# Kernel optimization log

Measured on AMD Instinct MI355X. Metric: run time of the kernel, lower is better.

## Reference

```python
import jax, jax.numpy as jnp
import numpy as np

SR = 32000
N_FFT = 1024
HOP = 320
N_MELS = 128
PCEN_EPS = 1e-6
LN_EPS = 1e-6


def _hz_to_mel(f):
    return 2595.0 * np.log10(1.0 + f / 700.0)


def _mel_to_hz(m):
    return 700.0 * (10.0 ** (m / 2595.0) - 1.0)


def make_mel_fb():
    # HTK-scale triangular mel filterbank, [n_freqs, n_mels] (torchaudio default)
    n_freqs = N_FFT // 2 + 1
    mels = np.linspace(_hz_to_mel(0.0), _hz_to_mel(SR / 2.0), N_MELS + 2)
    f_pts = _mel_to_hz(mels)                       # [n_mels+2]
    all_freqs = np.linspace(0.0, SR / 2.0, n_freqs)
    f_diff = f_pts[1:] - f_pts[:-1]
    slopes = f_pts[None, :] - all_freqs[:, None]   # [n_freqs, n_mels+2]
    down = -slopes[:, :-2] / f_diff[:-1]
    up = slopes[:, 2:] / f_diff[1:]
    fb = np.maximum(0.0, np.minimum(down, up))
    return fb.astype(np.float32)


def setup_inputs() -> dict:
    key = jax.random.key(0)
    x = jax.random.normal(key, (16, 320000), dtype=jnp.float32)
    return {
        "x": x,
        "mel_fb": jnp.asarray(make_mel_fb()),
        "log_s": jnp.asarray(np.log(0.025), dtype=jnp.float32),
        "log_alpha": jnp.asarray(np.log(0.98), dtype=jnp.float32),
        "log_delta": jnp.asarray(np.log(2.0), dtype=jnp.float32),
        "log_r": jnp.asarray(np.log(0.5), dtype=jnp.float32),
    }


def reference(x, mel_fb, log_s, log_alpha, log_delta, log_r):
    B, T = x.shape
    pad = N_FFT // 2
    xp = jnp.pad(x, ((0, 0), (pad, pad)), mode="reflect")
    n_frames = 1 + (xp.shape[1] - N_FFT) // HOP           # = T//HOP + 1
    idx = jnp.arange(n_frames)[:, None] * HOP + jnp.arange(N_FFT)[None, :]
    frames = xp[:, idx]                                    # [B, F, N_FFT]
    # periodic Hann window (torch.hann_window default)
    win = 0.5 * (1.0 - jnp.cos(2.0 * jnp.pi * jnp.arange(N_FFT) / N_FFT))
    spec = jnp.fft.rfft(frames * win, axis=-1)             # [B, F, N_FFT//2+1]
    power = spec.real ** 2 + spec.imag ** 2                # power spectrogram
    E = jnp.einsum("bfk,km->bfm", power, mel_fb)           # [B, F, M] mel energies

    s = jnp.exp(log_s)
    alpha = jnp.exp(log_alpha)
    delta = jnp.exp(log_delta)
    r = jnp.exp(log_r)

    # Causal exponential smoother M(t) = (1-s) M(t-1) + s E(t), M init = first frame
    E_t = jnp.swapaxes(E, 0, 1)                            # [F, B, M]

    def step(m, e):
        m = (1.0 - s) * m + s * e
        return m, m

    _, M_t = jax.lax.scan(step, E_t[0], E_t)
    smooth = jnp.swapaxes(M_t, 0, 1)                       # [B, F, M]

    pcen = (E / (PCEN_EPS + smooth) ** alpha + delta) ** r - delta ** r

    # affine-free layer_norm over last dim (n_mels), eps=1e-6
    mu = jnp.mean(pcen, axis=-1, keepdims=True)
    var = jnp.var(pcen, axis=-1, keepdims=True)
    return (pcen - mu) / jnp.sqrt(var + LN_EPS)
```

## Files before the change

kernel.cpp:

```cpp
#include <hip/hip_runtime.h>
#include <math.h>

#define SRATE   32000
#define NFFT    1024
#define HOP     320
#define NBINS   513
#define NMELS   128
#define NFRAMES 1001
#define NB      16
#define TLEN    320000
#define PCEN_EPS 1e-6f
#define LN_EPS   1e-6f
#define MAXW     64

#define CL      16
#define NCHUNK  63

__device__ __forceinline__ int P(int i) { return i + (i >> 3); }
#define ZPAD 1152

__global__ __launch_bounds__(256) void k_prep(
    const float* __restrict__ fb, int* __restrict__ kmin, int* __restrict__ klen,
    float* __restrict__ wv, float* __restrict__ win, float2* __restrict__ twg)
{
    const int blk = blockIdx.x;
    const int tid = threadIdx.x;
    if (blk < NMELS) {
        const int m = blk;
        __shared__ int smin[4], smax[4];
        int lmin = 1 << 30, lmax = -1;
        for (int k = tid; k < NBINS; k += 256) {
            if (fb[k * NMELS + m] > 0.f) {
                if (k < lmin) lmin = k;
                if (k > lmax) lmax = k;
            }
        }
        #pragma unroll
        for (int off = 32; off; off >>= 1) {
            int om = __shfl_xor(lmin, off); if (om < lmin) lmin = om;
            int ox = __shfl_xor(lmax, off); if (ox > lmax) lmax = ox;
        }
        if ((tid & 63) == 0) { smin[tid >> 6] = lmin; smax[tid >> 6] = lmax; }
        __syncthreads();
        int k0 = min(min(smin[0], smin[1]), min(smin[2], smin[3]));
        int k1 = max(max(smax[0], smax[1]), max(smax[2], smax[3]));
        int L  = (k1 < 0) ? 0 : min(k1 - k0 + 1, MAXW);
        if (tid == 0) { kmin[m] = (k1 < 0) ? 0 : k0; klen[m] = L; }
        if (tid < L) wv[m * MAXW + tid] = fb[(k0 + tid) * NMELS + m];
    } else {
        const int i = (blk - NMELS) * 256 + tid;
        if (i < NFFT) {
            float sp = sinpif((float)i * (1.0f / (float)NFFT));
            win[i] = sp * sp;
        } else if (i < NFFT + 256) {
            int n = i - NFFT;
            float sn, cn;
            sincospif((float)n * (1.0f / 512.0f), &sn, &cn);
            twg[n] = make_float2(cn, -sn);
        }
    }
}

__global__ __launch_bounds__(256, 4) void k_melspec(
    const float* __restrict__ x,
    const int*   __restrict__ kmin,
    const int*   __restrict__ klen,
    const float* __restrict__ wv,
    const float* __restrict__ fb,
    const float* __restrict__ win_g,
    const float2* __restrict__ twg,
    float* __restrict__ E,
    int usePacked)
{
    __shared__ float2 zA[2][ZPAD], zB[2][ZPAD];
    __shared__ float2 tws[256];

    const int tid = threadIdx.x;
    const int g   = blockIdx.x;

    if (usePacked) {
        tws[tid] = twg[tid];
    } else {
        float sn, cn;
        sincospif((float)tid * (1.0f / 512.0f), &sn, &cn);
        tws[tid] = make_float2(cn, -sn);
    }

    const int i0 = tid * 4;
    #pragma unroll
    for (int u = 0; u < 2; ++u) {
        const int fa = 4 * g + 2 * u;
        const int fbr = fa + 1;
        const int ba = fa / NFRAMES,  ta = fa  - ba * NFRAMES;
        const int bb = fbr / NFRAMES, tb = fbr - bb * NFRAMES;
        const float* xa = x + (size_t)ba * TLEN;
        const float* xb = x + (size_t)bb * TLEN;
        const int basea = ta * HOP - (NFFT / 2);
        const int baseb = tb * HOP - (NFFT / 2);
        const bool safe = usePacked &&
                          basea >= 0 && baseb >= 0 &&
                          (basea + NFFT - 1 < TLEN) && (baseb + NFFT - 1 < TLEN);
        if (safe) {
            float4 v0 = *(const float4*)(xa + basea + i0);
            float4 v1 = *(const float4*)(xb + baseb + i0);
            float4 w  = *(const float4*)(win_g + i0);
            zA[u][P(i0 + 0)] = make_float2(v0.x * w.x, v1.x * w.x);
            zA[u][P(i0 + 1)] = make_float2(v0.y * w.y, v1.y * w.y);
            zA[u][P(i0 + 2)] = make_float2(v0.z * w.z, v1.z * w.z);
            zA[u][P(i0 + 3)] = make_float2(v0.w * w.w, v1.w * w.w);
        } else {
            #pragma unroll
            for (int q = 0; q < 4; ++q) {
                const int i = i0 + q;
                int j0 = basea + i;
                j0 = (j0 < 0) ? -j0 : ((j0 >= TLEN) ? (2 * TLEN - 2 - j0) : j0);
                int j1 = baseb + i;
                j1 = (j1 < 0) ? -j1 : ((j1 >= TLEN) ? (2 * TLEN - 2 - j1) : j1);
                float w;
                if (usePacked) w = win_g[i];
                else { float sp = sinpif((float)i * (1.0f / (float)NFFT)); w = sp * sp; }
                zA[u][P(i)] = make_float2(xa[j0] * w, xb[j1] * w);
            }
        }
    }
    __syncthreads();

    float2 (*zs)[ZPAD] = zA;
    float2 (*zd)[ZPAD] = zB;
    #pragma unroll
    for (int st = 0; st < 5; ++st) {
        const int mm = 1 << (2 * st);
        const int n  = tid & ~(mm - 1);
        const int o  = (n << 2) | (tid & (mm - 1));
        float2 w1 = tws[n];
        const float c1 = w1.x, s1 = w1.y;
        const float c2 = c1 * c1 - s1 * s1, s2 = 2.f * c1 * s1;
        const float c3 = c1 * c2 - s1 * s2, s3 = c1 * s2 + s1 * c2;
        #pragma unroll
        for (int u = 0; u < 2; ++u) {
            float2 a0 = zs[u][P(tid)];
            float2 a1 = zs[u][P(tid + 256)];
            float2 a2 = zs[u][P(tid + 512)];
            float2 a3 = zs[u][P(tid + 768)];
            float t0r = a0.x + a2.x, t0i = a0.y + a2.y;
            float t1r = a0.x - a2.x, t1i = a0.y - a2.y;
            float t2r = a1.x + a3.x, t2i = a1.y + a3.y;
            float t3r = a1.y - a3.y, t3i = a3.x - a1.x;
            float y1r = t1r + t3r, y1i = t1i + t3i;
            float y2r = t0r - t2r, y2i = t0i - t2i;
            float y3r = t1r - t3r, y3i = t1i - t3i;
            zd[u][P(o)]          = make_float2(t0r + t2r,            t0i + t2i);
            zd[u][P(o + mm)]     = make_float2(y1r * c1 - y1i * s1,  y1r * s1 + y1i * c1);
            zd[u][P(o + 2 * mm)] = make_float2(y2r * c2 - y2i * s2,  y2r * s2 + y2i * c2);
            zd[u][P(o + 3 * mm)] = make_float2(y3r * c3 - y3i * s3,  y3r * s3 + y3i * c3);
        }
        __syncthreads();
        float2 (*tp)[ZPAD] = zs; zs = zd; zd = tp;
    }

    {
        const int u  = tid >> 7;
        const int kk = tid & 127;
        for (int k = kk; k < NBINS; k += 128) {
            float2 Z  = zs[u][P(k)];
            const int kr = (NFFT - k) & (NFFT - 1);
            float2 Zr = zs[u][P(kr)];
            float x1r = Z.x + Zr.x, x1i = Z.y - Zr.y;
            float x2r = Z.y + Zr.y, x2i = Zr.x - Z.x;
            zd[u][P(k)] = make_float2(0.25f * (x1r * x1r + x1i * x1i),
                                      0.25f * (x2r * x2r + x2i * x2i));
        }
    }
    __syncthreads();

    {
        const int u = tid >> 7;
        const int m = tid & 127;
        const int fa = 4 * g + 2 * u;
        float acc0 = 0.f, acc1 = 0.f;
        if (usePacked) {
            const int k0 = kmin[m], L = klen[m];
            const float* w = wv + m * MAXW;
            for (int j = 0; j < L; ++j) {
                float2 pk = zd[u][P(k0 + j)];
                float ww = w[j];
                acc0 += pk.x * ww; acc1 += pk.y * ww;
            }
        } else {
            for (int k = 0; k < NBINS; ++k) {
                float2 pk = zd[u][P(k)];
                float ww = fb[k * NMELS + m];
                acc0 += pk.x * ww; acc1 += pk.y * ww;
            }
        }
        E[(size_t)fa * NMELS + m]       = acc0;
        E[(size_t)(fa + 1) * NMELS + m] = acc1;
    }
}

__global__ __launch_bounds__(256) void k_pcen_chunk(
    const float* __restrict__ E, float* __restrict__ Bws,
    float* __restrict__ E0ws, const float* __restrict__ p_ls)
{
    const int gid = blockIdx.x * blockDim.x + threadIdx.x;
    const int m = gid & (NMELS - 1);
    const int c = (gid >> 7) % NCHUNK;
    const int b = gid / (NMELS * NCHUNK);

    const float s = expf(p_ls[0]);
    const float a = 1.f - s;

    const int t0 = c * CL;
    const int L  = (t0 + CL <= NFRAMES) ? CL : (NFRAMES - t0);
    const float* col = E + (size_t)b * NFRAMES * NMELS + m;

    if (c == 0) E0ws[b * NMELS + m] = col[0];

    float Bacc;
    if (L == CL) {
        float e[CL];
        #pragma unroll
        for (int j = 0; j < CL; ++j)
            e[j] = col[(size_t)(t0 + j) * NMELS];
        float p0 = 0.f, p1 = 0.f, p2 = 0.f, p3 = 0.f;
        #pragma unroll
        for (int u = 0; u < 4; ++u) {
            p0 = a * p0 + s * e[u];
            p1 = a * p1 + s * e[4 + u];
            p2 = a * p2 + s * e[8 + u];
            p3 = a * p3 + s * e[12 + u];
        }
        const float a2 = a * a, a4 = a2 * a2, a8 = a4 * a4, a12 = a8 * a4;
        Bacc = a12 * p0 + a8 * p1 + a4 * p2 + p3;
    } else {
        Bacc = 0.f;
        for (int j = 0; j < L; ++j)
            Bacc = a * Bacc + s * col[(size_t)(t0 + j) * NMELS];
    }
    Bws[gid] = Bacc;
}

__global__ __launch_bounds__(256) void k_pcen_ln(
    float* __restrict__ E, const float* __restrict__ Bws,
    const float* __restrict__ E0ws,
    const float* __restrict__ p_ls, const float* __restrict__ p_la,
    const float* __restrict__ p_ld, const float* __restrict__ p_lr)
{
    __shared__ float sm[2 * CL][NMELS];

    const int tid  = threadIdx.x;
    const int half = tid >> 7;
    const int m    = tid & 127;
    const int b    = blockIdx.x >> 5;
    const int cp   = blockIdx.x & 31;
    const int c    = cp * 2 + half;

    const float s     = expf(p_ls[0]);
    const float alpha = expf(p_la[0]);
    const float delta = expf(p_ld[0]);
    const float r     = expf(p_lr[0]);
    const float dr    = __powf(delta, r);
    const float a     = 1.f - s;
    const float a2 = a * a, a4 = a2 * a2, a8 = a4 * a4;
    const float a16 = a8 * a8;

    if (c < NCHUNK) {
        float M = E0ws[b * NMELS + m];
        const float* Bcol = Bws + (size_t)b * NCHUNK * NMELS + m;
        int cc = 0;
        for (; cc + 8 <= c; cc += 8) {
            float b0 = Bcol[(size_t)(cc + 0) * NMELS];
            float b1 = Bcol[(size_t)(cc + 1) * NMELS];
            float b2 = Bcol[(size_t)(cc + 2) * NMELS];
            float b3 = Bcol[(size_t)(cc + 3) * NMELS];
            float b4 = Bcol[(size_t)(cc + 4) * NMELS];
            float b5 = Bcol[(size_t)(cc + 5) * NMELS];
            float b6 = Bcol[(size_t)(cc + 6) * NMELS];
            float b7 = Bcol[(size_t)(cc + 7) * NMELS];
            M = a16 * M + b0; M = a16 * M + b1; M = a16 * M + b2; M = a16 * M + b3;
            M = a16 * M + b4; M = a16 * M + b5; M = a16 * M + b6; M = a16 * M + b7;
        }
        for (; cc < c; ++cc)
            M = a16 * M + Bcol[(size_t)cc * NMELS];

        const int t0 = c * CL;
        const int L  = (t0 + CL <= NFRAMES) ? CL : (NFRAMES - t0);
        const float* col = E + ((size_t)b * NFRAMES + t0) * NMELS + m;
        for (int j = 0; j < L; ++j) {
            float e = col[(size_t)j * NMELS];
            M = a * M + s * e;
            float den = __powf(PCEN_EPS + M, alpha);
            sm[half * CL + j][m] = __powf(e / den + delta, r) - dr;
        }
    }
    __syncthreads();

    const int wid  = tid >> 6;
    const int lane = tid & 63;
    for (int row = wid; row < 2 * CL; row += 4) {
        const int cc = cp * 2 + (row >> 4);
        if (cc >= NCHUNK) continue;
        const int j   = row & (CL - 1);
        const int tt0 = cc * CL;
        const int LL  = (tt0 + CL <= NFRAMES) ? CL : (NFRAMES - tt0);
        if (j >= LL) continue;
        float v0 = sm[row][lane], v1 = sm[row][lane + 64];
        float sum = v0 + v1;
        float sq  = v0 * v0 + v1 * v1;
        #pragma unroll
        for (int off = 32; off; off >>= 1) {
            sum += __shfl_xor(sum, off);
            sq  += __shfl_xor(sq,  off);
        }
        float mu  = sum * (1.f / 128.f);
        float var = sq * (1.f / 128.f) - mu * mu;
        float inv = rsqrtf(var + LN_EPS);
        float* p = E + ((size_t)b * NFRAMES + tt0 + j) * NMELS;
        p[lane]      = (v0 - mu) * inv;
        p[lane + 64] = (v1 - mu) * inv;
    }
}

__global__ __launch_bounds__(256) void k_pcen_serial(
    float* __restrict__ E,
    const float* __restrict__ p_ls, const float* __restrict__ p_la,
    const float* __restrict__ p_ld, const float* __restrict__ p_lr)
{
    const int gid = blockIdx.x * blockDim.x + threadIdx.x;
    const int b = gid >> 7;
    const int m = gid & 127;

    const float s     = expf(p_ls[0]);
    const float alpha = expf(p_la[0]);
    const float delta = expf(p_ld[0]);
    const float r     = expf(p_lr[0]);
    const float dr    = powf(delta, r);
    const float a     = 1.f - s;

    float* col = E + (size_t)b * NFRAMES * NMELS + m;
    float M = col[0];
    for (int t = 0; t < NFRAMES; ++t) {
        float e = col[(size_t)t * NMELS];
        M = a * M + s * e;
        float den = __powf(PCEN_EPS + M, alpha);
        float p   = __powf(e / den + delta, r) - dr;
        col[(size_t)t * NMELS] = p;
    }
}

__global__ __launch_bounds__(256) void k_ln(float* __restrict__ out) {
    const int wid  = threadIdx.x >> 6;
    const int lane = threadIdx.x & 63;
    const int row  = blockIdx.x * 4 + wid;
    float* p = out + (size_t)row * NMELS;
    float v0 = p[lane], v1 = p[lane + 64];
    float sum = v0 + v1;
    float sq  = v0 * v0 + v1 * v1;
    #pragma unroll
    for (int off = 32; off; off >>= 1) {
        sum += __shfl_xor(sum, off);
        sq  += __shfl_xor(sq,  off);
    }
    float mu  = sum * (1.f / 128.f);
    float var = sq * (1.f / 128.f) - mu * mu;
    float inv = rsqrtf(var + LN_EPS);
    p[lane]      = (v0 - mu) * inv;
    p[lane + 64] = (v1 - mu) * inv;
}

extern "C" void kernel_launch(void* const* d_in, const int* in_sizes, int n_in,
                              void* d_out, int out_size, void* d_ws, size_t ws_size,
                              hipStream_t stream) {
    const float* x   = (const float*)d_in[0];
    const float* fb  = (const float*)d_in[1];
    const float* lsp = (const float*)d_in[2];
    const float* lap = (const float*)d_in[3];
    const float* ldp = (const float*)d_in[4];
    const float* lrp = (const float*)d_in[5];
    float* out = (float*)d_out;

    const size_t packElems = 128 + 128 + 8192 + 1024 + 512;
    const size_t scanElems = (size_t)NB * NCHUNK * NMELS;
    const size_t needPack  = packElems * 4;
    const size_t needScan  = (packElems + scanElems + (size_t)NB * NMELS) * 4;

    int usePacked = (ws_size >= needPack) ? 1 : 0;
    int useScan   = (ws_size >= needScan) ? 1 : 0;

    int*    kmin = (int*)d_ws;
    int*    klen = kmin + NMELS;
    float*  wv   = (float*)(klen + NMELS);
    float*  win  = wv + (size_t)NMELS * MAXW;
    float2* twg  = (float2*)(win + NFFT);
    float*  Bws  = (float*)(twg + 256);
    float*  E0ws = Bws + scanElems;

    if (usePacked)
        k_prep<<<NMELS + 5, 256, 0, stream>>>(fb, kmin, klen, wv, win, twg);

    k_melspec<<<NB * NFRAMES / 4, 256, 0, stream>>>(
        x, kmin, klen, wv, fb, win, twg, out, usePacked);

    if (useScan) {
        const int nThread = NB * NCHUNK * NMELS;
        k_pcen_chunk<<<nThread / 256, 256, 0, stream>>>(out, Bws, E0ws, lsp);
        k_pcen_ln<<<NB * 32, 256, 0, stream>>>(out, Bws, E0ws, lsp, lap, ldp, lrp);
    } else {
        k_pcen_serial<<<(NB * NMELS) / 256, 256, 0, stream>>>(out, lsp, lap, ldp, lrp);
        k_ln<<<(NB * NFRAMES) / 4, 256, 0, stream>>>(out);
    }
}
```

Before: 82.30 us.

## Use in-place radix-4 DIF FFT with digit-reversal table to halve LDS

Replaces the out-of-place Stockham radix-4 FFT, which ping-ponged between two shared buffers, with an in-place decimation-in-frequency FFT on a single buffer. The last stage is split out because it needs no twiddles. A shared lookup table maps natural bin indices to the digit-reversed padded LDS positions for the real-split and mel stages. Halving the FFT shared memory lets launch bounds ask for 7 blocks per CU instead of 4, aiming to hide latency. The cost is an extra table build per block and indirect LDS reads during the post-processing and mel accumulation.

```diff
diff --git a/kernel.cpp b/kernel.cpp
--- a/kernel.cpp
+++ b/kernel.cpp
@@ -18,6 +18,11 @@
 
 __device__ __forceinline__ int P(int i) { return i + (i >> 3); }
 #define ZPAD 1152
+
+__device__ __forceinline__ int DR4(int e) {
+    return ((e & 3) << 8) | (((e >> 2) & 3) << 6) | (((e >> 4) & 3) << 4)
+         | (((e >> 6) & 3) << 2) | ((e >> 8) & 3);
+}
 
 __global__ __launch_bounds__(256) void k_prep(
     const float* __restrict__ fb, int* __restrict__ kmin, int* __restrict__ klen,
@@ -61,7 +66,7 @@
     }
 }
 
-__global__ __launch_bounds__(256, 4) void k_melspec(
+__global__ __launch_bounds__(256, 7) void k_melspec(
     const float* __restrict__ x,
     const int*   __restrict__ kmin,
     const int*   __restrict__ klen,
@@ -72,8 +77,9 @@
     float* __restrict__ E,
     int usePacked)
 {
-    __shared__ float2 zA[2][ZPAD], zB[2][ZPAD];
+    __shared__ float2 z[2][ZPAD];
     __shared__ float2 tws[256];
+    __shared__ unsigned short prt[1024];
 
     const int tid = threadIdx.x;
     const int g   = blockIdx.x;
@@ -85,6 +91,9 @@
         sincospif((float)tid * (1.0f / 512.0f), &sn, &cn);
         tws[tid] = make_float2(cn, -sn);
     }
+    #pragma unroll
+    for (int e = tid; e < 1024; e += 256)
+        prt[e] = (unsigned short)P(DR4(e));
 
     const int i0 = tid * 4;
     #pragma unroll
@@ -104,10 +113,10 @@
             float4 v0 = *(const float4*)(xa + basea + i0);
             float4 v1 = *(const float4*)(xb + baseb + i0);
             float4 w  = *(const float4*)(win_g + i0);
-            zA[u][P(i0 + 0)] = make_float2(v0.x * w.x, v1.x * w.x);
-            zA[u][P(i0 + 1)] = make_float2(v0.y * w.y, v1.y * w.y);
-            zA[u][P(i0 + 2)] = make_float2(v0.z * w.z, v1.z * w.z);
-            zA[u][P(i0 + 3)] = make_float2(v0.w * w.w, v1.w * w.w);
+            z[u][P(i0 + 0)] = make_float2(v0.x * w.x, v1.x * w.x);
+            z[u][P(i0 + 1)] = make_float2(v0.y * w.y, v1.y * w.y);
+            z[u][P(i0 + 2)] = make_float2(v0.z * w.z, v1.z * w.z);
+            z[u][P(i0 + 3)] = make_float2(v0.w * w.w, v1.w * w.w);
         } else {
             #pragma unroll
             for (int q = 0; q < 4; ++q) {
@@ -119,29 +128,28 @@
                 float w;
                 if (usePacked) w = win_g[i];
                 else { float sp = sinpif((float)i * (1.0f / (float)NFFT)); w = sp * sp; }
-                zA[u][P(i)] = make_float2(xa[j0] * w, xb[j1] * w);
+                z[u][P(i)] = make_float2(xa[j0] * w, xb[j1] * w);
             }
         }
     }
     __syncthreads();
 
-    float2 (*zs)[ZPAD] = zA;
-    float2 (*zd)[ZPAD] = zB;
     #pragma unroll
-    for (int st = 0; st < 5; ++st) {
-        const int mm = 1 << (2 * st);
-        const int n  = tid & ~(mm - 1);
-        const int o  = (n << 2) | (tid & (mm - 1));
+    for (int s = 0; s < 4; ++s) {
+        const int q    = 256 >> (2 * s);
+        const int k    = tid & (q - 1);
+        const int base = ((tid & ~(q - 1)) << 2) | k;
+        const int n    = k << (2 * s);
         float2 w1 = tws[n];
         const float c1 = w1.x, s1 = w1.y;
         const float c2 = c1 * c1 - s1 * s1, s2 = 2.f * c1 * s1;
         const float c3 = c1 * c2 - s1 * s2, s3 = c1 * s2 + s1 * c2;
         #pragma unroll
         for (int u = 0; u < 2; ++u) {
-            float2 a0 = zs[u][P(tid)];
-            float2 a1 = zs[u][P(tid + 256)];
-            float2 a2 = zs[u][P(tid + 512)];
-            float2 a3 = zs[u][P(tid + 768)];
+            float2 a0 = z[u][P(base)];
+            float2 a1 = z[u][P(base + q)];
+            float2 a2 = z[u][P(base + 2 * q)];
+            float2 a3 = z[u][P(base + 3 * q)];
             float t0r = a0.x + a2.x, t0i = a0.y + a2.y;
             float t1r = a0.x - a2.x, t1i = a0.y - a2.y;
             float t2r = a1.x + a3.x, t2i = a1.y + a3.y;
@@ -149,26 +157,46 @@
             float y1r = t1r + t3r, y1i = t1i + t3i;
             float y2r = t0r - t2r, y2i = t0i - t2i;
             float y3r = t1r - t3r, y3i = t1i - t3i;
-            zd[u][P(o)]          = make_float2(t0r + t2r,            t0i + t2i);
-            zd[u][P(o + mm)]     = make_float2(y1r * c1 - y1i * s1,  y1r * s1 + y1i * c1);
-            zd[u][P(o + 2 * mm)] = make_float2(y2r * c2 - y2i * s2,  y2r * s2 + y2i * c2);
-            zd[u][P(o + 3 * mm)] = make_float2(y3r * c3 - y3i * s3,  y3r * s3 + y3i * c3);
+            z[u][P(base)]         = make_float2(t0r + t2r,           t0i + t2i);
+            z[u][P(base + q)]     = make_float2(y1r * c1 - y1i * s1, y1r * s1 + y1i * c1);
+            z[u][P(base + 2 * q)] = make_float2(y2r * c2 - y2i * s2, y2r * s2 + y2i * c2);
+            z[u][P(base + 3 * q)] = make_float2(y3r * c3 - y3i * s3, y3r * s3 + y3i * c3);
         }
         __syncthreads();
-        float2 (*tp)[ZPAD] = zs; zs = zd; zd = tp;
+    }
+
+    {
+        const int base = tid << 2;
+        #pragma unroll
+        for (int u = 0; u < 2; ++u) {
+            float2 a0 = z[u][P(base)];
+            float2 a1 = z[u][P(base + 1)];
+            float2 a2 = z[u][P(base + 2)];
+            float2 a3 = z[u][P(base + 3)];
+            float t0r = a0.x + a2.x, t0i = a0.y + a2.y;
+            float t1r = a0.x - a2.x, t1i = a0.y - a2.y;
+            float t2r = a1.x + a3.x, t2i = a1.y + a3.y;
+            float t3r = a1.y - a3.y, t3i = a3.x - a1.x;
+            z[u][P(base)]     = make_float2(t0r + t2r, t0i + t2i);
+            z[u][P(base + 1)] = make_float2(t1r + t3r, t1i + t3i);
+            z[u][P(base + 2)] = make_float2(t0r - t2r, t0i - t2i);
+            z[u][P(base + 3)] = make_float2(t1r - t3r, t1i - t3i);
+        }
+        __syncthreads();
     }
 
     {
         const int u  = tid >> 7;
         const int kk = tid & 127;
-        for (int k = kk; k < NBINS; k += 128) {
-            float2 Z  = zs[u][P(k)];
-            const int kr = (NFFT - k) & (NFFT - 1);
-            float2 Zr = zs[u][P(kr)];
+        for (int k = kk; k < 513; k += 128) {
+            const int sk  = prt[k];
+            const int skr = prt[(NFFT - k) & (NFFT - 1)];
+            float2 Z  = z[u][sk];
+            float2 Zr = z[u][skr];
             float x1r = Z.x + Zr.x, x1i = Z.y - Zr.y;
             float x2r = Z.y + Zr.y, x2i = Zr.x - Z.x;
-            zd[u][P(k)] = make_float2(0.25f * (x1r * x1r + x1i * x1i),
-                                      0.25f * (x2r * x2r + x2i * x2i));
+            z[u][sk] = make_float2(0.25f * (x1r * x1r + x1i * x1i),
+                                   0.25f * (x2r * x2r + x2i * x2i));
         }
     }
     __syncthreads();
@@ -182,13 +210,13 @@
             const int k0 = kmin[m], L = klen[m];
             const float* w = wv + m * MAXW;
             for (int j = 0; j < L; ++j) {
-                float2 pk = zd[u][P(k0 + j)];
+                float2 pk = z[u][prt[k0 + j]];
                 float ww = w[j];
                 acc0 += pk.x * ww; acc1 += pk.y * ww;
             }
         } else {
             for (int k = 0; k < NBINS; ++k) {
-                float2 pk = zd[u][P(k)];
+                float2 pk = z[u][prt[k]];
                 float ww = fb[k * NMELS + m];
                 acc0 += pk.x * ww; acc1 += pk.y * ww;
             }
```

New measurement: 84.70 us. +2.9%, slower.

## Compute each FFT pair per wavefront with register radix-16 stages and swizzled LDS

Applied to the files above, without the earlier changes.

The 5-stage block-wide radix-4 FFT with a __syncthreads after every stage is replaced by a per-wavefront 1024-point FFT. Each 64-lane wave owns one frame pair and does two register-resident radix-16 passes plus a final radix-4 pass, using an XOR-swizzled LDS layout and a precomputed permutation table for bit-reversed output. Each block now handles 8 frames instead of 4, and block-level barriers are removed in favour of implicit wave-synchronous execution. The removed barriers rely on lockstep within a 64-wide wave with no explicit wave barrier, so correctness depends on compiler ordering of LDS accesses. Register pressure from the 16-element arrays may also limit occupancy.

```diff
diff --git a/kernel.cpp b/kernel.cpp
--- a/kernel.cpp
+++ b/kernel.cpp
@@ -16,8 +16,53 @@
 #define CL      16
 #define NCHUNK  63
 
-__device__ __forceinline__ int P(int i) { return i + (i >> 3); }
-#define ZPAD 1152
+__device__ __forceinline__ int SWZ(int i) {
+    return i ^ (((i >> 6) & 3) << 2) ^ ((i >> 4) & 3);
+}
+
+__device__ __forceinline__ float2 cmul(float2 a, float2 b) {
+    return make_float2(a.x * b.x - a.y * b.y, a.x * b.y + a.y * b.x);
+}
+
+__device__ __forceinline__ void r4(float2 a0, float2 a1, float2 a2, float2 a3,
+                                   float2& y0, float2& y1, float2& y2, float2& y3) {
+    float t0r = a0.x + a2.x, t0i = a0.y + a2.y;
+    float t1r = a0.x - a2.x, t1i = a0.y - a2.y;
+    float t2r = a1.x + a3.x, t2i = a1.y + a3.y;
+    float t3r = a1.y - a3.y, t3i = a3.x - a1.x;
+    y0 = make_float2(t0r + t2r, t0i + t2i);
+    y1 = make_float2(t1r + t3r, t1i + t3i);
+    y2 = make_float2(t0r - t2r, t0i - t2i);
+    y3 = make_float2(t1r - t3r, t1i - t3i);
+}
+
+__device__ __forceinline__ void fft16(float2* x) {
+    const float2 W1  = make_float2( 0.92387953f, -0.38268343f);
+    const float2 W2  = make_float2( 0.70710678f, -0.70710678f);
+    const float2 W3  = make_float2( 0.38268343f, -0.92387953f);
+    const float2 W6  = make_float2(-0.70710678f, -0.70710678f);
+    const float2 W9  = make_float2(-0.92387953f,  0.38268343f);
+    float2 v[4][4];
+    {
+        float2 g0, g1, g2, g3;
+        r4(x[0], x[4], x[8], x[12], g0, g1, g2, g3);
+        v[0][0] = g0; v[1][0] = g1; v[2][0] = g2; v[3][0] = g3;
+        r4(x[1], x[5], x[9], x[13], g0, g1, g2, g3);
+        v[0][1] = g0; v[1][1] = cmul(g1, W1); v[2][1] = cmul(g2, W2); v[3][1] = cmul(g3, W3);
+        r4(x[2], x[6], x[10], x[14], g0, g1, g2, g3);
+        v[0][2] = g0; v[1][2] = cmul(g1, W2);
+        v[2][2] = make_float2(g2.y, -g2.x);
+        v[3][2] = cmul(g3, W6);
+        r4(x[3], x[7], x[11], x[15], g0, g1, g2, g3);
+        v[0][3] = g0; v[1][3] = cmul(g1, W3); v[2][3] = cmul(g2, W6); v[3][3] = cmul(g3, W9);
+    }
+    #pragma unroll
+    for (int p2 = 0; p2 < 4; ++p2) {
+        float2 y0, y1, y2, y3;
+        r4(v[p2][0], v[p2][1], v[p2][2], v[p2][3], y0, y1, y2, y3);
+        x[p2] = y0; x[p2 + 4] = y1; x[p2 + 8] = y2; x[p2 + 12] = y3;
+    }
+}
 
 __global__ __launch_bounds__(256) void k_prep(
     const float* __restrict__ fb, int* __restrict__ kmin, int* __restrict__ klen,
@@ -72,27 +117,32 @@
     float* __restrict__ E,
     int usePacked)
 {
-    __shared__ float2 zA[2][ZPAD], zB[2][ZPAD];
-    __shared__ float2 tws[256];
-
-    const int tid = threadIdx.x;
-    const int g   = blockIdx.x;
+    __shared__ float2 z[4][1024];
+    __shared__ float2 tws_sh[64];
+    __shared__ unsigned short prt[513];
+
+    const int tid  = threadIdx.x;
+    const int w    = tid >> 6;
+    const int lane = tid & 63;
+    const int g    = blockIdx.x;
+    float2* T = z[w];
 
     if (usePacked) {
-        tws[tid] = twg[tid];
+        tws_sh[lane] = twg[lane];
     } else {
         float sn, cn;
-        sincospif((float)tid * (1.0f / 512.0f), &sn, &cn);
-        tws[tid] = make_float2(cn, -sn);
-    }
-
-    const int i0 = tid * 4;
-    #pragma unroll
-    for (int u = 0; u < 2; ++u) {
-        const int fa = 4 * g + 2 * u;
-        const int fbr = fa + 1;
+        sincospif((float)lane * (1.0f / 512.0f), &sn, &cn);
+        tws_sh[lane] = make_float2(cn, -sn);
+    }
+    for (int k = lane; k <= 512; k += 64) {
+        const int sl = 64 * (k & 15) + 4 * ((k >> 4) & 15) + (k >> 8);
+        prt[k] = (unsigned short)SWZ(sl);
+    }
+
+    {
+        const int fa = 8 * g + 2 * w, fbf = fa + 1;
         const int ba = fa / NFRAMES,  ta = fa  - ba * NFRAMES;
-        const int bb = fbr / NFRAMES, tb = fbr - bb * NFRAMES;
+        const int bb = fbf / NFRAMES, tb = fbf - bb * NFRAMES;
         const float* xa = x + (size_t)ba * TLEN;
         const float* xb = x + (size_t)bb * TLEN;
         const int basea = ta * HOP - (NFFT / 2);
@@ -101,100 +151,108 @@
                           basea >= 0 && baseb >= 0 &&
                           (basea + NFFT - 1 < TLEN) && (baseb + NFFT - 1 < TLEN);
         if (safe) {
-            float4 v0 = *(const float4*)(xa + basea + i0);
-            float4 v1 = *(const float4*)(xb + baseb + i0);
-            float4 w  = *(const float4*)(win_g + i0);
-            zA[u][P(i0 + 0)] = make_float2(v0.x * w.x, v1.x * w.x);
-            zA[u][P(i0 + 1)] = make_float2(v0.y * w.y, v1.y * w.y);
-            zA[u][P(i0 + 2)] = make_float2(v0.z * w.z, v1.z * w.z);
-            zA[u][P(i0 + 3)] = make_float2(v0.w * w.w, v1.w * w.w);
-        } else {
             #pragma unroll
             for (int q = 0; q < 4; ++q) {
-                const int i = i0 + q;
+                const int i0 = 4 * lane + 256 * q;
+                float4 v0 = *(const float4*)(xa + basea + i0);
+                float4 v1 = *(const float4*)(xb + baseb + i0);
+                float4 ww = *(const float4*)(win_g + i0);
+                T[SWZ(i0 + 0)] = make_float2(v0.x * ww.x, v1.x * ww.x);
+                T[SWZ(i0 + 1)] = make_float2(v0.y * ww.y, v1.y * ww.y);
+                T[SWZ(i0 + 2)] = make_float2(v0.z * ww.z, v1.z * ww.z);
+                T[SWZ(i0 + 3)] = make_float2(v0.w * ww.w, v1.w * ww.w);
+            }
+        } else {
+            for (int i = lane; i < NFFT; i += 64) {
                 int j0 = basea + i;
                 j0 = (j0 < 0) ? -j0 : ((j0 >= TLEN) ? (2 * TLEN - 2 - j0) : j0);
                 int j1 = baseb + i;
                 j1 = (j1 < 0) ? -j1 : ((j1 >= TLEN) ? (2 * TLEN - 2 - j1) : j1);
-                float w;
-                if (usePacked) w = win_g[i];
-                else { float sp = sinpif((float)i * (1.0f / (float)NFFT)); w = sp * sp; }
-                zA[u][P(i)] = make_float2(xa[j0] * w, xb[j1] * w);
+                float ww;
+                if (usePacked) ww = win_g[i];
+                else { float sp = sinpif((float)i * (1.0f / (float)NFFT)); ww = sp * sp; }
+                T[SWZ(i)] = make_float2(xa[j0] * ww, xb[j1] * ww);
             }
         }
     }
-    __syncthreads();
-
-    float2 (*zs)[ZPAD] = zA;
-    float2 (*zd)[ZPAD] = zB;
+
+    float2 xr[16];
+
+    {
+        #pragma unroll
+        for (int q = 0; q < 16; ++q) xr[q] = T[SWZ(lane + 64 * q)];
+        fft16(xr);
+        const float2 w1 = tws_sh[lane];
+        float2 wp = w1;
+        T[SWZ(lane)] = xr[0];
+        #pragma unroll
+        for (int p = 1; p < 16; ++p) {
+            T[SWZ(lane + 64 * p)] = cmul(xr[p], wp);
+            wp = cmul(wp, w1);
+        }
+    }
+
+    {
+        const int p1 = lane >> 2, jj = lane & 3;
+        const int base = 64 * p1 + jj;
+        #pragma unroll
+        for (int q = 0; q < 16; ++q) xr[q] = T[SWZ(base + 4 * q)];
+        fft16(xr);
+        const float2 w1 = tws_sh[16 * jj];
+        float2 wp = w1;
+        T[SWZ(base)] = xr[0];
+        #pragma unroll
+        for (int p = 1; p < 16; ++p) {
+            T[SWZ(base + 4 * p)] = cmul(xr[p], wp);
+            wp = cmul(wp, w1);
+        }
+    }
+
     #pragma unroll
-    for (int st = 0; st < 5; ++st) {
-        const int mm = 1 << (2 * st);
-        const int n  = tid & ~(mm - 1);
-        const int o  = (n << 2) | (tid & (mm - 1));
-        float2 w1 = tws[n];
-        const float c1 = w1.x, s1 = w1.y;
-        const float c2 = c1 * c1 - s1 * s1, s2 = 2.f * c1 * s1;
-        const float c3 = c1 * c2 - s1 * s2, s3 = c1 * s2 + s1 * c2;
-        #pragma unroll
-        for (int u = 0; u < 2; ++u) {
-            float2 a0 = zs[u][P(tid)];
-            float2 a1 = zs[u][P(tid + 256)];
-            float2 a2 = zs[u][P(tid + 512)];
-            float2 a3 = zs[u][P(tid + 768)];
-            float t0r = a0.x + a2.x, t0i = a0.y + a2.y;
-            float t1r = a0.x - a2.x, t1i = a0.y - a2.y;
-            float t2r = a1.x + a3.x, t2i = a1.y + a3.y;
-            float t3r = a1.y - a3.y, t3i = a3.x - a1.x;
-            float y1r = t1r + t3r, y1i = t1i + t3i;
-            float y2r = t0r - t2r, y2i = t0i - t2i;
-            float y3r = t1r - t3r, y3i = t1i - t3i;
-            zd[u][P(o)]          = make_float2(t0r + t2r,            t0i + t2i);
-            zd[u][P(o + mm)]     = make_float2(y1r * c1 - y1i * s1,  y1r * s1 + y1i * c1);
-            zd[u][P(o + 2 * mm)] = make_float2(y2r * c2 - y2i * s2,  y2r * s2 + y2i * c2);
-            zd[u][P(o + 3 * mm)] = make_float2(y3r * c3 - y3i * s3,  y3r * s3 + y3i * c3);
-        }
-        __syncthreads();
-        float2 (*tp)[ZPAD] = zs; zs = zd; zd = tp;
+    for (int h = 0; h < 4; ++h) {
+        const int b4 = 4 * (lane + 64 * h);
+        float2 a0 = T[SWZ(b4)], a1 = T[SWZ(b4 + 1)], a2 = T[SWZ(b4 + 2)], a3 = T[SWZ(b4 + 3)];
+        float2 y0, y1, y2, y3;
+        r4(a0, a1, a2, a3, y0, y1, y2, y3);
+        T[SWZ(b4)] = y0; T[SWZ(b4 + 1)] = y1; T[SWZ(b4 + 2)] = y2; T[SWZ(b4 + 3)] = y3;
+    }
+
+    for (int k = lane; k <= 512; k += 64) {
+        const int sk = prt[k];
+        const int kr = (NFFT - k) & (NFFT - 1);
+        const int slr = SWZ(64 * (kr & 15) + 4 * ((kr >> 4) & 15) + (kr >> 8));
+        float2 Z  = T[sk];
+        float2 Zr = T[slr];
+        float x1r = Z.x + Zr.x, x1i = Z.y - Zr.y;
+        float x2r = Z.y + Zr.y, x2i = Zr.x - Z.x;
+        T[sk] = make_float2(0.25f * (x1r * x1r + x1i * x1i),
+                            0.25f * (x2r * x2r + x2i * x2i));
     }
 
     {
-        const int u  = tid >> 7;
-        const int kk = tid & 127;
-        for (int k = kk; k < NBINS; k += 128) {
-            float2 Z  = zs[u][P(k)];
-            const int kr = (NFFT - k) & (NFFT - 1);
-            float2 Zr = zs[u][P(kr)];
-            float x1r = Z.x + Zr.x, x1i = Z.y - Zr.y;
-            float x2r = Z.y + Zr.y, x2i = Zr.x - Z.x;
-            zd[u][P(k)] = make_float2(0.25f * (x1r * x1r + x1i * x1i),
-                                      0.25f * (x2r * x2r + x2i * x2i));
-        }
-    }
-    __syncthreads();
-
-    {
-        const int u = tid >> 7;
-        const int m = tid & 127;
-        const int fa = 4 * g + 2 * u;
-        float acc0 = 0.f, acc1 = 0.f;
-        if (usePacked) {
-            const int k0 = kmin[m], L = klen[m];
-            const float* w = wv + m * MAXW;
-            for (int j = 0; j < L; ++j) {
-                float2 pk = zd[u][P(k0 + j)];
-                float ww = w[j];
-                acc0 += pk.x * ww; acc1 += pk.y * ww;
+        const int f0 = 8 * g + 2 * w;
+        #pragma unroll
+        for (int h = 0; h < 2; ++h) {
+            const int m = lane + 64 * h;
+            float acc0 = 0.f, acc1 = 0.f;
+            if (usePacked) {
+                const int k0 = kmin[m], L = klen[m];
+                const float* wz = wv + m * MAXW;
+                for (int j = 0; j < L; ++j) {
+                    float2 pk = T[prt[k0 + j]];
+                    float ww = wz[j];
+                    acc0 += pk.x * ww; acc1 += pk.y * ww;
+                }
+            } else {
+                for (int k = 0; k < NBINS; ++k) {
+                    float2 pk = T[prt[k]];
+                    float ww = fb[k * NMELS + m];
+                    acc0 += pk.x * ww; acc1 += pk.y * ww;
+                }
             }
-        } else {
-            for (int k = 0; k < NBINS; ++k) {
-                float2 pk = zd[u][P(k)];
-                float ww = fb[k * NMELS + m];
-                acc0 += pk.x * ww; acc1 += pk.y * ww;
-            }
-        }
-        E[(size_t)fa * NMELS + m]       = acc0;
-        E[(size_t)(fa + 1) * NMELS + m] = acc1;
+            E[(size_t)f0 * NMELS + m]       = acc0;
+            E[(size_t)(f0 + 1) * NMELS + m] = acc1;
+        }
     }
 }
 
@@ -398,7 +456,7 @@
     if (usePacked)
         k_prep<<<NMELS + 5, 256, 0, stream>>>(fb, kmin, klen, wv, win, twg);
 
-    k_melspec<<<NB * NFRAMES / 4, 256, 0, stream>>>(
+    k_melspec<<<NB * NFRAMES / 8, 256, 0, stream>>>(
         x, kmin, klen, wv, fb, win, twg, out, usePacked);
 
     if (useScan) {
```

Measured after the change: 78.82 us. 1.04x faster.
